# Optimization experiments

Hardware: AMD Instinct MI355X
Metric: run time of the kernel (lower is better)

Reference implementation:

```python
import jax, jax.numpy as jnp
import numpy as np
import math

B, S, QD, KD, LD, H = 32, 8192, 256, 256, 256, 8
SD = LD // H  # split_dim = 32

def setup_inputs() -> dict:
    key = jax.random.key(0)
    ks = jax.random.split(key, 8)
    query = jax.random.normal(ks[0], (B, QD), dtype=jnp.float32)
    keys = jax.random.normal(ks[1], (B, S, KD), dtype=jnp.float32)
    # binary padding mask: 1 = keep, 0 = pad
    padding_mask = (jax.random.uniform(ks[2], (B, 1, 1, S)) > 0.1).astype(jnp.float32)
    s = 1.0 / math.sqrt(KD)
    Wq = jax.random.normal(ks[3], (LD, QD), dtype=jnp.float32) * s
    Wk = jax.random.normal(ks[4], (LD, KD), dtype=jnp.float32) * s
    Wv = jax.random.normal(ks[5], (LD, KD), dtype=jnp.float32) * s
    Wu = jax.random.normal(ks[6], (LD, LD), dtype=jnp.float32) * (1.0 / math.sqrt(LD))
    bu = jnp.zeros((LD,), dtype=jnp.float32)
    return {"query": query, "keys": keys, "padding_mask": padding_mask,
            "Wq": Wq, "Wk": Wk, "Wv": Wv, "Wu": Wu, "bu": bu}

def reference(query, keys, padding_mask, Wq, Wk, Wv, Wu, bu):
    attn_mask_penalty = -10000.0
    b, s, _ = keys.shape
    # projections (torch Linear: x @ W.T)
    q = query @ Wq.T                      # (b, LD)
    k = keys @ Wk.T                       # (b, s, LD)
    v = keys @ Wv.T                       # (b, s, LD)
    q = q.reshape(b, H, SD)               # single query per head
    k = k.reshape(b, s, H, SD)
    v = v.reshape(b, s, H, SD)
    # scores: (b, H, 1, s)
    dot = jnp.einsum('bhd,bshd->bhs', q, k) / math.sqrt(SD)
    dot = dot[:, :, None, :]              # (b, H, 1, s)
    unmasked = dot
    masked = dot + (1.0 - padding_mask) * attn_mask_penalty
    attn = jax.nn.softmax(masked, axis=-1)  # (b, H, 1, s)
    out = jnp.einsum('bhs,bshd->bhd', attn[:, :, 0, :], v)  # (b, H, SD)
    out = out.reshape(b, H * SD)
    unified = out @ Wu.T + bu             # (b, LD)
    return (unified, unmasked)
```

## Files before the change

kernel.cpp:

```cpp
#include <hip/hip_runtime.h>

#define B_   32
#define S_   8192
#define C_   256
#define LD_  256
#define H_   8
#define SD_  32
#define NCH  32
#define CH   256

#define WS_QK    0
#define WS_LSUM  (WS_QK + B_*H_*C_)
#define WS_CTX   (WS_LSUM + B_*H_)
#define WS_TOTAL (WS_CTX + B_*H_*C_)

__global__ __launch_bounds__(256) void proj_qk(const float* __restrict__ query,
                                               const float* __restrict__ Wq,
                                               const float* __restrict__ Wk,
                                               float* __restrict__ ws) {
    const int b = blockIdx.x, t = threadIdx.x;
    __shared__ float qry[C_];
    __shared__ float qv[LD_];
    qry[t] = query[b * C_ + t];
    __syncthreads();
    {
        const float* wr = Wq + t * C_;
        float a = 0.f;
        for (int c = 0; c < C_; c += 4) {
            float4 w = *(const float4*)(wr + c);
            float4 x = *(const float4*)(qry + c);
            a = fmaf(w.x, x.x, fmaf(w.y, x.y, fmaf(w.z, x.z, fmaf(w.w, x.w, a))));
        }
        qv[t] = a;
    }
    __syncthreads();
    const float scale = 0.17677669529663687f;
    float* qkb = ws + WS_QK + b * H_ * C_;
    #pragma unroll
    for (int h = 0; h < H_; h++) {
        float a = 0.f;
        #pragma unroll 8
        for (int d = 0; d < SD_; d++) {
            a = fmaf(qv[h * SD_ + d], Wk[(h * SD_ + d) * C_ + t], a);
        }
        qkb[h * C_ + t] = a * scale;
    }
}

__global__ __launch_bounds__(256) void attn_pass(const float* __restrict__ keys,
                                                 const float* __restrict__ pmask,
                                                 const float* __restrict__ ws_qk,
                                                 float* __restrict__ lsum,
                                                 float* __restrict__ ctxsum,
                                                 float* __restrict__ out_unmasked) {
    const int b = blockIdx.y, ch = blockIdx.x, t = threadIdx.x;
    const int s0 = ch * CH;
    __shared__ float qk_s[H_ * C_];
    __shared__ float p_s[CH][H_];
    __shared__ float red[256];

    const float pm  = __builtin_nontemporal_load(pmask + b * S_ + s0 + t);

    const float* qkb = ws_qk + b * H_ * C_;
    for (int i = t; i < H_ * C_; i += 256) qk_s[i] = qkb[i];
    __syncthreads();

    const float* krow = keys + ((size_t)(b * S_) + s0 + t) * C_;
    float acc0 = 0.f, acc1 = 0.f, acc2 = 0.f, acc3 = 0.f;
    float acc4 = 0.f, acc5 = 0.f, acc6 = 0.f, acc7 = 0.f;
    for (int c = 0; c < C_; c += 4) {
        float4 kv = *(const float4*)(krow + c);
        float4 w0 = *(const float4*)(qk_s + 0 * C_ + c);
        float4 w1 = *(const float4*)(qk_s + 1 * C_ + c);
        float4 w2 = *(const float4*)(qk_s + 2 * C_ + c);
        float4 w3 = *(const float4*)(qk_s + 3 * C_ + c);
        float4 w4 = *(const float4*)(qk_s + 4 * C_ + c);
        float4 w5 = *(const float4*)(qk_s + 5 * C_ + c);
        float4 w6 = *(const float4*)(qk_s + 6 * C_ + c);
        float4 w7 = *(const float4*)(qk_s + 7 * C_ + c);
        acc0 = fmaf(kv.x, w0.x, fmaf(kv.y, w0.y, fmaf(kv.z, w0.z, fmaf(kv.w, w0.w, acc0))));
        acc1 = fmaf(kv.x, w1.x, fmaf(kv.y, w1.y, fmaf(kv.z, w1.z, fmaf(kv.w, w1.w, acc1))));
        acc2 = fmaf(kv.x, w2.x, fmaf(kv.y, w2.y, fmaf(kv.z, w2.z, fmaf(kv.w, w2.w, acc2))));
        acc3 = fmaf(kv.x, w3.x, fmaf(kv.y, w3.y, fmaf(kv.z, w3.z, fmaf(kv.w, w3.w, acc3))));
        acc4 = fmaf(kv.x, w4.x, fmaf(kv.y, w4.y, fmaf(kv.z, w4.z, fmaf(kv.w, w4.w, acc4))));
        acc5 = fmaf(kv.x, w5.x, fmaf(kv.y, w5.y, fmaf(kv.z, w5.z, fmaf(kv.w, w5.w, acc5))));
        acc6 = fmaf(kv.x, w6.x, fmaf(kv.y, w6.y, fmaf(kv.z, w6.z, fmaf(kv.w, w6.w, acc6))));
        acc7 = fmaf(kv.x, w7.x, fmaf(kv.y, w7.y, fmaf(kv.z, w7.z, fmaf(kv.w, w7.w, acc7))));
    }
    float* ub = out_unmasked + (size_t)b * H_ * S_ + s0 + t;
    __builtin_nontemporal_store(acc0, ub + 0 * S_);
    __builtin_nontemporal_store(acc1, ub + 1 * S_);
    __builtin_nontemporal_store(acc2, ub + 2 * S_);
    __builtin_nontemporal_store(acc3, ub + 3 * S_);
    __builtin_nontemporal_store(acc4, ub + 4 * S_);
    __builtin_nontemporal_store(acc5, ub + 5 * S_);
    __builtin_nontemporal_store(acc6, ub + 6 * S_);
    __builtin_nontemporal_store(acc7, ub + 7 * S_);
    const float pen = (1.0f - pm) * -10000.0f;
    float4 pv0 = make_float4(__expf(acc0 + pen), __expf(acc1 + pen),
                             __expf(acc2 + pen), __expf(acc3 + pen));
    float4 pv1 = make_float4(__expf(acc4 + pen), __expf(acc5 + pen),
                             __expf(acc6 + pen), __expf(acc7 + pen));
    *(float4*)&p_s[t][0] = pv0;
    *(float4*)&p_s[t][4] = pv1;
    __syncthreads();

    {
        const int h = t & 7, idx = t >> 3;
        float part = 0.f;
        #pragma unroll
        for (int i = 0; i < CH / 32; i++) part += p_s[idx + i * 32][h];
        red[t] = part;
    }
    __syncthreads();
    if (t < H_) {
        float tot = 0.f;
        #pragma unroll 8
        for (int idx = 0; idx < 32; idx++) tot += red[idx * 8 + t];
        atomicAdd(&lsum[b * H_ + t], tot);
    }

    float f0 = 0.f, f1 = 0.f, f2 = 0.f, f3 = 0.f, f4 = 0.f, f5 = 0.f, f6 = 0.f, f7 = 0.f;
    const float* kcol = keys + ((size_t)(b * S_) + s0) * C_ + t;
    #pragma unroll 8
    for (int s = CH - 1; s >= 0; s--) {
        float kv = kcol[(size_t)s * C_];
        float4 p0 = *(const float4*)&p_s[s][0];
        float4 p1 = *(const float4*)&p_s[s][4];
        f0 = fmaf(p0.x, kv, f0); f1 = fmaf(p0.y, kv, f1);
        f2 = fmaf(p0.z, kv, f2); f3 = fmaf(p0.w, kv, f3);
        f4 = fmaf(p1.x, kv, f4); f5 = fmaf(p1.y, kv, f5);
        f6 = fmaf(p1.z, kv, f6); f7 = fmaf(p1.w, kv, f7);
    }
    float* cb = ctxsum + (size_t)b * H_ * C_ + t;
    atomicAdd(cb + 0 * C_, f0); atomicAdd(cb + 1 * C_, f1);
    atomicAdd(cb + 2 * C_, f2); atomicAdd(cb + 3 * C_, f3);
    atomicAdd(cb + 4 * C_, f4); atomicAdd(cb + 5 * C_, f5);
    atomicAdd(cb + 6 * C_, f6); atomicAdd(cb + 7 * C_, f7);
}

__global__ __launch_bounds__(256) void finalize(const float* __restrict__ Wv,
                                                const float* __restrict__ Wu,
                                                const float* __restrict__ bu,
                                                const float* __restrict__ lsum,
                                                const float* __restrict__ ctxsum,
                                                float* __restrict__ out_unified) {
    const int b = blockIdx.x, t = threadIdx.x;
    __shared__ float ctxn[H_ * C_];
    __shared__ float outv[LD_];
    __shared__ float linv[H_];
    if (t < H_) linv[t] = 1.0f / lsum[b * H_ + t];
    __syncthreads();
    for (int i = t; i < H_ * C_; i += 256)
        ctxn[i] = ctxsum[(size_t)b * H_ * C_ + i] * linv[i >> 8];
    __syncthreads();
    {
        const float* wr = Wv + t * C_;
        const float* cx = ctxn + (t >> 5) * C_;
        float a = 0.f;
        for (int c = 0; c < C_; c += 4) {
            float4 w = *(const float4*)(wr + c);
            float4 x = *(const float4*)(cx + c);
            a = fmaf(w.x, x.x, fmaf(w.y, x.y, fmaf(w.z, x.z, fmaf(w.w, x.w, a))));
        }
        outv[t] = a;
    }
    __syncthreads();
    {
        const float* wr = Wu + t * C_;
        float a = bu[t];
        for (int c = 0; c < C_; c += 4) {
            float4 w = *(const float4*)(wr + c);
            float4 x = *(const float4*)(outv + c);
            a = fmaf(w.x, x.x, fmaf(w.y, x.y, fmaf(w.z, x.z, fmaf(w.w, x.w, a))));
        }
        out_unified[b * LD_ + t] = a;
    }
}

extern "C" void kernel_launch(void* const* d_in, const int* in_sizes, int n_in,
                              void* d_out, int out_size, void* d_ws, size_t ws_size,
                              hipStream_t stream) {
    const float* query = (const float*)d_in[0];
    const float* keys  = (const float*)d_in[1];
    const float* pmask = (const float*)d_in[2];
    const float* Wq    = (const float*)d_in[3];
    const float* Wk    = (const float*)d_in[4];
    const float* Wv    = (const float*)d_in[5];
    const float* Wu    = (const float*)d_in[6];
    const float* bu    = (const float*)d_in[7];

    float* out          = (float*)d_out;
    float* out_unified  = out;
    float* out_unmasked = out + B_ * LD_;
    float* ws           = (float*)d_ws;

    hipMemsetAsync(ws + WS_LSUM, 0, (size_t)(B_ * H_ + B_ * H_ * C_) * sizeof(float), stream);

    proj_qk<<<B_, 256, 0, stream>>>(query, Wq, Wk, ws);

    dim3 gridB(NCH, B_);
    attn_pass<<<gridB, 256, 0, stream>>>(keys, pmask, ws + WS_QK,
                                         ws + WS_LSUM, ws + WS_CTX, out_unmasked);

    finalize<<<B_, 256, 0, stream>>>(Wv, Wu, bu, ws + WS_LSUM, ws + WS_CTX, out_unified);
}
```

Baseline: 472.6 us.

## Shrink attention chunks and split score dot products across channel quarters

Sequence chunks shrink from 256 to 64 rows, so the grid grows to 128x32 blocks. Each of four thread groups computes partial scores over a quarter of the channels, and the partials are reduced through shared memory. The per-head exp sums are reduced with wave shuffles. The aim is more parallelism and occupancy, and a score-phase access pattern in which adjacent threads read less-strided key rows. In exchange there are four times as many atomic adds into the context and lsum buffers, and more shared-memory traffic.

```diff
diff --git a/kernel.cpp b/kernel.cpp
--- a/kernel.cpp
+++ b/kernel.cpp
@@ -6,8 +6,8 @@
 #define LD_  256
 #define H_   8
 #define SD_  32
-#define NCH  32
-#define CH   256
+#define CH   64
+#define NCH  (S_ / CH)
 
 #define WS_QK    0
 #define WS_LSUM  (WS_QK + B_*H_*C_)
@@ -55,88 +55,99 @@
                                                  float* __restrict__ out_unmasked) {
     const int b = blockIdx.y, ch = blockIdx.x, t = threadIdx.x;
     const int s0 = ch * CH;
-    __shared__ float qk_s[H_ * C_];
-    __shared__ float p_s[CH][H_];
-    __shared__ float red[256];
-
-    const float pm  = __builtin_nontemporal_load(pmask + b * S_ + s0 + t);
-
-    const float* qkb = ws_qk + b * H_ * C_;
-    for (int i = t; i < H_ * C_; i += 256) qk_s[i] = qkb[i];
-    __syncthreads();
-
-    const float* krow = keys + ((size_t)(b * S_) + s0 + t) * C_;
-    float acc0 = 0.f, acc1 = 0.f, acc2 = 0.f, acc3 = 0.f;
-    float acc4 = 0.f, acc5 = 0.f, acc6 = 0.f, acc7 = 0.f;
-    for (int c = 0; c < C_; c += 4) {
-        float4 kv = *(const float4*)(krow + c);
-        float4 w0 = *(const float4*)(qk_s + 0 * C_ + c);
-        float4 w1 = *(const float4*)(qk_s + 1 * C_ + c);
-        float4 w2 = *(const float4*)(qk_s + 2 * C_ + c);
-        float4 w3 = *(const float4*)(qk_s + 3 * C_ + c);
-        float4 w4 = *(const float4*)(qk_s + 4 * C_ + c);
-        float4 w5 = *(const float4*)(qk_s + 5 * C_ + c);
-        float4 w6 = *(const float4*)(qk_s + 6 * C_ + c);
-        float4 w7 = *(const float4*)(qk_s + 7 * C_ + c);
-        acc0 = fmaf(kv.x, w0.x, fmaf(kv.y, w0.y, fmaf(kv.z, w0.z, fmaf(kv.w, w0.w, acc0))));
-        acc1 = fmaf(kv.x, w1.x, fmaf(kv.y, w1.y, fmaf(kv.z, w1.z, fmaf(kv.w, w1.w, acc1))));
-        acc2 = fmaf(kv.x, w2.x, fmaf(kv.y, w2.y, fmaf(kv.z, w2.z, fmaf(kv.w, w2.w, acc2))));
-        acc3 = fmaf(kv.x, w3.x, fmaf(kv.y, w3.y, fmaf(kv.z, w3.z, fmaf(kv.w, w3.w, acc3))));
-        acc4 = fmaf(kv.x, w4.x, fmaf(kv.y, w4.y, fmaf(kv.z, w4.z, fmaf(kv.w, w4.w, acc4))));
-        acc5 = fmaf(kv.x, w5.x, fmaf(kv.y, w5.y, fmaf(kv.z, w5.z, fmaf(kv.w, w5.w, acc5))));
-        acc6 = fmaf(kv.x, w6.x, fmaf(kv.y, w6.y, fmaf(kv.z, w6.z, fmaf(kv.w, w6.w, acc6))));
-        acc7 = fmaf(kv.x, w7.x, fmaf(kv.y, w7.y, fmaf(kv.z, w7.z, fmaf(kv.w, w7.w, acc7))));
-    }
-    float* ub = out_unmasked + (size_t)b * H_ * S_ + s0 + t;
-    __builtin_nontemporal_store(acc0, ub + 0 * S_);
-    __builtin_nontemporal_store(acc1, ub + 1 * S_);
-    __builtin_nontemporal_store(acc2, ub + 2 * S_);
-    __builtin_nontemporal_store(acc3, ub + 3 * S_);
-    __builtin_nontemporal_store(acc4, ub + 4 * S_);
-    __builtin_nontemporal_store(acc5, ub + 5 * S_);
-    __builtin_nontemporal_store(acc6, ub + 6 * S_);
-    __builtin_nontemporal_store(acc7, ub + 7 * S_);
-    const float pen = (1.0f - pm) * -10000.0f;
-    float4 pv0 = make_float4(__expf(acc0 + pen), __expf(acc1 + pen),
-                             __expf(acc2 + pen), __expf(acc3 + pen));
-    float4 pv1 = make_float4(__expf(acc4 + pen), __expf(acc5 + pen),
-                             __expf(acc6 + pen), __expf(acc7 + pen));
-    *(float4*)&p_s[t][0] = pv0;
-    *(float4*)&p_s[t][4] = pv1;
-    __syncthreads();
-
-    {
-        const int h = t & 7, idx = t >> 3;
-        float part = 0.f;
+    __shared__ float qk_s[H_][C_];
+    __shared__ float part[4][H_][CH];
+    __shared__ float p_t[CH][H_];
+    __shared__ float pm_s[CH];
+
+    {
+        const float4* src = (const float4*)(ws_qk + b * H_ * C_);
+        float4* dst = (float4*)&qk_s[0][0];
+        dst[t]       = src[t];
+        dst[t + 256] = src[t + 256];
+    }
+    if (t < CH) pm_s[t] = __builtin_nontemporal_load(pmask + b * S_ + s0 + t);
+    __syncthreads();
+
+    {
+        const int sl = t & 63, q = t >> 6;
+        const float* krow = keys + ((size_t)b * S_ + s0 + sl) * C_ + q * 64;
+        const float* qrow = &qk_s[0][q * 64];
+        float acc0 = 0.f, acc1 = 0.f, acc2 = 0.f, acc3 = 0.f;
+        float acc4 = 0.f, acc5 = 0.f, acc6 = 0.f, acc7 = 0.f;
         #pragma unroll
-        for (int i = 0; i < CH / 32; i++) part += p_s[idx + i * 32][h];
-        red[t] = part;
-    }
-    __syncthreads();
-    if (t < H_) {
-        float tot = 0.f;
-        #pragma unroll 8
-        for (int idx = 0; idx < 32; idx++) tot += red[idx * 8 + t];
-        atomicAdd(&lsum[b * H_ + t], tot);
-    }
-
-    float f0 = 0.f, f1 = 0.f, f2 = 0.f, f3 = 0.f, f4 = 0.f, f5 = 0.f, f6 = 0.f, f7 = 0.f;
-    const float* kcol = keys + ((size_t)(b * S_) + s0) * C_ + t;
-    #pragma unroll 8
-    for (int s = CH - 1; s >= 0; s--) {
-        float kv = kcol[(size_t)s * C_];
-        float4 p0 = *(const float4*)&p_s[s][0];
-        float4 p1 = *(const float4*)&p_s[s][4];
-        f0 = fmaf(p0.x, kv, f0); f1 = fmaf(p0.y, kv, f1);
-        f2 = fmaf(p0.z, kv, f2); f3 = fmaf(p0.w, kv, f3);
-        f4 = fmaf(p1.x, kv, f4); f5 = fmaf(p1.y, kv, f5);
-        f6 = fmaf(p1.z, kv, f6); f7 = fmaf(p1.w, kv, f7);
-    }
-    float* cb = ctxsum + (size_t)b * H_ * C_ + t;
-    atomicAdd(cb + 0 * C_, f0); atomicAdd(cb + 1 * C_, f1);
-    atomicAdd(cb + 2 * C_, f2); atomicAdd(cb + 3 * C_, f3);
-    atomicAdd(cb + 4 * C_, f4); atomicAdd(cb + 5 * C_, f5);
-    atomicAdd(cb + 6 * C_, f6); atomicAdd(cb + 7 * C_, f7);
+        for (int c = 0; c < 64; c += 4) {
+            float4 kv = *(const float4*)(krow + c);
+            float4 w0 = *(const float4*)(qrow + 0 * C_ + c);
+            float4 w1 = *(const float4*)(qrow + 1 * C_ + c);
+            float4 w2 = *(const float4*)(qrow + 2 * C_ + c);
+            float4 w3 = *(const float4*)(qrow + 3 * C_ + c);
+            float4 w4 = *(const float4*)(qrow + 4 * C_ + c);
+            float4 w5 = *(const float4*)(qrow + 5 * C_ + c);
+            float4 w6 = *(const float4*)(qrow + 6 * C_ + c);
+            float4 w7 = *(const float4*)(qrow + 7 * C_ + c);
+            acc0 = fmaf(kv.x, w0.x, fmaf(kv.y, w0.y, fmaf(kv.z, w0.z, fmaf(kv.w, w0.w, acc0))));
+            acc1 = fmaf(kv.x, w1.x, fmaf(kv.y, w1.y, fmaf(kv.z, w1.z, fmaf(kv.w, w1.w, acc1))));
+            acc2 = fmaf(kv.x, w2.x, fmaf(kv.y, w2.y, fmaf(kv.z, w2.z, fmaf(kv.w, w2.w, acc2))));
+            acc3 = fmaf(kv.x, w3.x, fmaf(kv.y, w3.y, fmaf(kv.z, w3.z, fmaf(kv.w, w3.w, acc3))));
+            acc4 = fmaf(kv.x, w4.x, fmaf(kv.y, w4.y, fmaf(kv.z, w4.z, fmaf(kv.w, w4.w, acc4))));
+            acc5 = fmaf(kv.x, w5.x, fmaf(kv.y, w5.y, fmaf(kv.z, w5.z, fmaf(kv.w, w5.w, acc5))));
+            acc6 = fmaf(kv.x, w6.x, fmaf(kv.y, w6.y, fmaf(kv.z, w6.z, fmaf(kv.w, w6.w, acc6))));
+            acc7 = fmaf(kv.x, w7.x, fmaf(kv.y, w7.y, fmaf(kv.z, w7.z, fmaf(kv.w, w7.w, acc7))));
+        }
+        part[q][0][sl] = acc0; part[q][1][sl] = acc1;
+        part[q][2][sl] = acc2; part[q][3][sl] = acc3;
+        part[q][4][sl] = acc4; part[q][5][sl] = acc5;
+        part[q][6][sl] = acc6; part[q][7][sl] = acc7;
+    }
+    __syncthreads();
+
+    {
+        const int s = t & 63, g = t >> 6;
+        const int h0 = 2 * g, h1 = 2 * g + 1;
+        const float pen = (1.0f - pm_s[s]) * -10000.0f;
+        float d0 = part[0][h0][s] + part[1][h0][s] + part[2][h0][s] + part[3][h0][s];
+        float d1 = part[0][h1][s] + part[1][h1][s] + part[2][h1][s] + part[3][h1][s];
+        float* ub = out_unmasked + (size_t)(b * H_) * S_ + s0 + s;
+        __builtin_nontemporal_store(d0, ub + (size_t)h0 * S_);
+        __builtin_nontemporal_store(d1, ub + (size_t)h1 * S_);
+        float p0 = __expf(d0 + pen);
+        float p1 = __expf(d1 + pen);
+        p_t[s][h0] = p0;
+        p_t[s][h1] = p1;
+        float r0 = p0, r1 = p1;
+        #pragma unroll
+        for (int off = 32; off > 0; off >>= 1) {
+            r0 += __shfl_xor(r0, off);
+            r1 += __shfl_xor(r1, off);
+        }
+        if (s == 0) {
+            atomicAdd(&lsum[b * H_ + h0], r0);
+            atomicAdd(&lsum[b * H_ + h1], r1);
+        }
+    }
+    __syncthreads();
+
+    {
+        float f0 = 0.f, f1 = 0.f, f2 = 0.f, f3 = 0.f;
+        float f4 = 0.f, f5 = 0.f, f6 = 0.f, f7 = 0.f;
+        const float* kcol = keys + ((size_t)b * S_ + s0) * C_ + t;
+        #pragma unroll 4
+        for (int s = 0; s < CH; ++s) {
+            float kv = kcol[(size_t)s * C_];
+            float4 pA = *(const float4*)&p_t[s][0];
+            float4 pB = *(const float4*)&p_t[s][4];
+            f0 = fmaf(pA.x, kv, f0); f1 = fmaf(pA.y, kv, f1);
+            f2 = fmaf(pA.z, kv, f2); f3 = fmaf(pA.w, kv, f3);
+            f4 = fmaf(pB.x, kv, f4); f5 = fmaf(pB.y, kv, f5);
+            f6 = fmaf(pB.z, kv, f6); f7 = fmaf(pB.w, kv, f7);
+        }
+        float* cb = ctxsum + (size_t)b * H_ * C_ + t;
+        atomicAdd(cb + 0 * C_, f0); atomicAdd(cb + 1 * C_, f1);
+        atomicAdd(cb + 2 * C_, f2); atomicAdd(cb + 3 * C_, f3);
+        atomicAdd(cb + 4 * C_, f4); atomicAdd(cb + 5 * C_, f5);
+        atomicAdd(cb + 6 * C_, f6); atomicAdd(cb + 7 * C_, f7);
+    }
 }
 
 __global__ __launch_bounds__(256) void finalize(const float* __restrict__ Wv,
```

New measurement: 541.9 us. 14.7% more time.
